# Kernel tuning notes

Measured on AMD Instinct MI355X. Metric: run time of the kernel, lower is better.

## Reference

```python
import jax, jax.numpy as jnp
import numpy as np

N, E, D, L = 50000, 640000, 128, 3  # nodes, edges, channels, layers
EPS = 1e-5


def setup_inputs() -> dict:
    key = jax.random.key(0)
    ks = jax.random.split(key, 10)
    s = 1.0 / np.sqrt(D)
    inp = {
        "x": jax.random.normal(ks[0], (N, D), dtype=jnp.float32),
        "edge_attr": jax.random.normal(ks[1], (E, D), dtype=jnp.float32),
        "w_self": jax.random.normal(ks[2], (L, D, D), dtype=jnp.float32) * s,
        "b_self": jnp.zeros((L, D), dtype=jnp.float32),
        "w_in": jax.random.normal(ks[3], (L, D, D), dtype=jnp.float32) * s,
        "b_in": jnp.zeros((L, D), dtype=jnp.float32),
        "w_rel": jax.random.normal(ks[4], (L, D, D), dtype=jnp.float32) * s,
        "b_rel": jnp.zeros((L, D), dtype=jnp.float32),
        "bn_gamma": jnp.ones((L - 1, D), dtype=jnp.float32),
        "bn_beta": jnp.zeros((L - 1, D), dtype=jnp.float32),
        "edge_index": jax.random.randint(ks[5], (2, E), 0, N, dtype=jnp.int64),
    }
    return inp


def _batchnorm(h, gamma, beta):
    mu = jnp.mean(h, axis=0)
    var = jnp.mean(jnp.square(h - mu), axis=0)  # biased var (torch BN training)
    return (h - mu) * jax.lax.rsqrt(var + EPS) * gamma + beta


def reference(x, edge_attr, w_self, b_self, w_in, b_in, w_rel, b_rel,
              bn_gamma, bn_beta, edge_index):
    src, dst = edge_index[0], edge_index[1]
    # per-node in-degree for mean aggregation (zero-degree nodes -> 0)
    cnt = jax.ops.segment_sum(jnp.ones((E, 1), x.dtype), dst, num_segments=N)
    denom = jnp.maximum(cnt, 1.0)
    for i in range(L):
        # message: lin_in(x_j * edge_attr)
        msg = jnp.einsum('ed,fd->ef', x[src] * edge_attr, w_in[i]) + b_in[i]
        agg = jax.ops.segment_sum(msg, dst, num_segments=N) / denom  # scatter-mean
        x = agg + jnp.einsum('nd,fd->nf', x, w_self[i]) + b_self[i]
        edge_attr = jnp.einsum('ed,fd->ef', edge_attr, w_rel[i]) + b_rel[i]
        if i < L - 1:
            x = jax.nn.relu(_batchnorm(x, bn_gamma[i], bn_beta[i]))
            # dropout p=0.0 -> identity
    return (x, edge_attr)
```

## Files before the change

kernel.cpp:

```cpp
#include <hip/hip_runtime.h>

#define DD 128

typedef __attribute__((ext_vector_type(8))) short bf16x8;
typedef __attribute__((ext_vector_type(4))) short bf16x4;
typedef __attribute__((ext_vector_type(4))) float f32x4;
typedef unsigned short u16;

__device__ __forceinline__ unsigned short f2bf(float f) {
  union { float f; unsigned u; } v; v.f = f;
  unsigned u = v.u;
  return (unsigned short)((u + 0x7FFFu + ((u >> 16) & 1u)) >> 16);
}
__device__ __forceinline__ float bf2f(unsigned short h) {
  union { unsigned u; float f; } v; v.u = ((unsigned)h) << 16; return v.f;
}

__device__ __forceinline__ bf16x8 pack8(f32x4 a, f32x4 b) {
  bf16x8 r;
  r[0] = (short)f2bf(a.x); r[1] = (short)f2bf(a.y);
  r[2] = (short)f2bf(a.z); r[3] = (short)f2bf(a.w);
  r[4] = (short)f2bf(b.x); r[5] = (short)f2bf(b.y);
  r[6] = (short)f2bf(b.z); r[7] = (short)f2bf(b.w);
  return r;
}

__device__ __forceinline__ bool idx_is64(const int* p) {
  return (p[1] | p[3] | p[5] | p[7]) == 0;
}
__device__ __forceinline__ int ld_idx(const int* p, long long i, bool is64) {
  return is64 ? (int)((const long long*)p)[i] : p[i];
}

__global__ void k_count(const int* __restrict__ idx, int* __restrict__ cnt, int E) {
  int e = blockIdx.x * blockDim.x + threadIdx.x;
  if (e >= E) return;
  bool is64 = idx_is64(idx);
  int d = ld_idx(idx, (long long)E + e, is64);
  atomicAdd(&cnt[d], 1);
}

__global__ __launch_bounds__(1024) void k_scan(const int* __restrict__ cnt,
    int* __restrict__ row_start, int* __restrict__ cursor, int N) {
  __shared__ int part[1024];
  int t = threadIdx.x;
  int chunk = (N + 1023) >> 10;
  int lo = t * chunk, hi = lo + chunk; if (hi > N) hi = N; if (lo > N) lo = N;
  int s = 0;
  for (int i = lo; i < hi; ++i) s += cnt[i];
  part[t] = s;
  __syncthreads();
  for (int off = 1; off < 1024; off <<= 1) {
    int v = (t >= off) ? part[t - off] : 0;
    __syncthreads();
    part[t] += v;
    __syncthreads();
  }
  int run = (t == 0) ? 0 : part[t - 1];
  for (int i = lo; i < hi; ++i) {
    row_start[i] = run; cursor[i] = run; run += cnt[i];
  }
  if (t == 1023) row_start[N] = part[1023];
}

__global__ void k_fill(const int* __restrict__ idx, int* __restrict__ cursor,
                       int* __restrict__ edge_of, int* __restrict__ src_csr, int E) {
  int e = blockIdx.x * blockDim.x + threadIdx.x;
  if (e >= E) return;
  bool is64 = idx_is64(idx);
  int s = ld_idx(idx, e, is64);
  int d = ld_idx(idx, (long long)E + e, is64);
  int pos = atomicAdd(&cursor[d], 1);
  edge_of[pos] = e;
  src_csr[pos] = s;
}

__global__ __launch_bounds__(256) void k_agg0(const float* __restrict__ x,
    const float* __restrict__ ea, const int* __restrict__ edge_of,
    const int* __restrict__ src_csr, const int* __restrict__ row_start,
    float* __restrict__ aggm, u16* __restrict__ eaC) {
  int n = blockIdx.x * 4 + (threadIdx.x >> 6);
  int lane = threadIdx.x & 63;
  int esub = lane >> 4, cg = lane & 15;
  int c0 = cg * 8;
  int s0 = row_start[n], s1 = row_start[n + 1];
  int len = s1 - s0;
  float acc[8];
#pragma unroll
  for (int j = 0; j < 8; ++j) acc[j] = 0.f;
  for (int kk = 0; kk < len; kk += 4) {
    int kx = kk + esub;
    bool act = kx < len;
    int k = s0 + (act ? kx : 0);
    int e = edge_of[k];
    int sn = src_csr[k];
    f32x4 e0 = *(const f32x4*)(ea + (size_t)e * DD + c0);
    f32x4 e1 = *(const f32x4*)(ea + (size_t)e * DD + c0 + 4);
    f32x4 x0 = *(const f32x4*)(x + (size_t)sn * DD + c0);
    f32x4 x1 = *(const f32x4*)(x + (size_t)sn * DD + c0 + 4);
    if (act) {
      *(bf16x8*)(eaC + (size_t)k * DD + c0) = pack8(e0, e1);
#pragma unroll
      for (int j = 0; j < 4; ++j) acc[j] += x0[j] * e0[j];
#pragma unroll
      for (int j = 0; j < 4; ++j) acc[4 + j] += x1[j] * e1[j];
    }
  }
  float inv = (len > 0) ? 1.0f / (float)len : 0.0f;
#pragma unroll
  for (int j = 0; j < 8; ++j) {
    float s = acc[j];
    s += __shfl_xor(s, 16);
    s += __shfl_xor(s, 32);
    acc[j] = s * inv;
  }
  if (esub == 0) {
    f32x4 lo, hi;
#pragma unroll
    for (int j = 0; j < 4; ++j) { lo[j] = acc[j]; hi[j] = acc[4 + j]; }
    *(f32x4*)(aggm + (size_t)n * DD + c0) = lo;
    *(f32x4*)(aggm + (size_t)n * DD + c0 + 4) = hi;
  }
}

__global__ __launch_bounds__(256) void k_aggN(const u16* __restrict__ xb,
    const u16* __restrict__ eaC, const int* __restrict__ src_csr,
    const int* __restrict__ row_start, const float* __restrict__ scale,
    const float* __restrict__ shift, float* __restrict__ aggm) {
  int n = blockIdx.x * 4 + (threadIdx.x >> 6);
  int lane = threadIdx.x & 63;
  int esub = lane >> 4, cg = lane & 15;
  int c0 = cg * 8;
  float sc[8], sh[8];
#pragma unroll
  for (int j = 0; j < 8; ++j) { sc[j] = scale[c0 + j]; sh[j] = shift[c0 + j]; }
  int s0 = row_start[n], s1 = row_start[n + 1];
  int len = s1 - s0;
  float acc[8];
#pragma unroll
  for (int j = 0; j < 8; ++j) acc[j] = 0.f;
  for (int kk = 0; kk < len; kk += 4) {
    int kx = kk + esub;
    bool act = kx < len;
    int k = s0 + (act ? kx : 0);
    int sn = src_csr[k];
    bf16x8 ev = *(const bf16x8*)(eaC + (size_t)k * DD + c0);
    bf16x8 xv = *(const bf16x8*)(xb + (size_t)sn * DD + c0);
    if (act) {
#pragma unroll
      for (int j = 0; j < 8; ++j) {
        float xf = fmaxf(bf2f((u16)xv[j]) * sc[j] + sh[j], 0.f);
        acc[j] += xf * bf2f((u16)ev[j]);
      }
    }
  }
  float inv = (len > 0) ? 1.0f / (float)len : 0.0f;
#pragma unroll
  for (int j = 0; j < 8; ++j) {
    float s = acc[j];
    s += __shfl_xor(s, 16);
    s += __shfl_xor(s, 32);
    acc[j] = s * inv;
  }
  if (esub == 0) {
    f32x4 lo, hi;
#pragma unroll
    for (int j = 0; j < 4; ++j) { lo[j] = acc[j]; hi[j] = acc[4 + j]; }
    *(f32x4*)(aggm + (size_t)n * DD + c0) = lo;
    *(f32x4*)(aggm + (size_t)n * DD + c0 + 4) = hi;
  }
}

template <typename TX, bool BN, typename TO, bool STATS>
__global__ __launch_bounds__(256) void k_node(const float* __restrict__ aggm,
    const TX* __restrict__ xc, const float* __restrict__ W_in,
    const float* __restrict__ W_self, const float* __restrict__ b_in,
    const float* __restrict__ b_self, const int* __restrict__ row_start,
    const float* __restrict__ scale, const float* __restrict__ shift,
    TO* __restrict__ xn, float* __restrict__ gsum, float* __restrict__ gssq,
    int ntiles) {
  __shared__ short Wl[DD * 256];
  for (int q = threadIdx.x; q < DD * 256 / 4; q += 256) {
    int off = q * 4;
    int f = off >> 8, k = off & 255;
    f32x4 w = (k < 128) ? *(const f32x4*)(W_in + f * 128 + k)
                        : *(const f32x4*)(W_self + f * 128 + (k - 128));
    unsigned byte = ((unsigned)(f * 512 + k * 2)) ^ (unsigned)((f & 7) << 4);
    bf16x4 s4;
    s4[0] = (short)f2bf(w.x); s4[1] = (short)f2bf(w.y);
    s4[2] = (short)f2bf(w.z); s4[3] = (short)f2bf(w.w);
    *(bf16x4*)((char*)Wl + byte) = s4;
  }
  __syncthreads();
  int wave = threadIdx.x >> 6, lane = threadIdx.x & 63;
  int tile = blockIdx.x * 4 + wave;
  if (tile >= ntiles) return;
  int r = lane & 15, g = lane >> 4;
  int arowi = tile * 16 + r;
  const float* arow = aggm + (size_t)arowi * DD;
  const TX* xrow = xc + (size_t)arowi * DD;
  bf16x8 a[8];
#pragma unroll
  for (int ks = 0; ks < 4; ++ks) {
    const float* p = arow + ks * 32 + g * 8;
    a[ks] = pack8(*(const f32x4*)p, *(const f32x4*)(p + 4));
  }
#pragma unroll
  for (int ks = 0; ks < 4; ++ks) {
    int c0 = ks * 32 + g * 8;
    float v[8];
    if constexpr (sizeof(TX) == 2) {
      bf16x8 raw = *(const bf16x8*)(xrow + c0);
#pragma unroll
      for (int j = 0; j < 8; ++j) v[j] = bf2f((u16)raw[j]);
    } else {
      f32x4 r0 = *(const f32x4*)((const float*)xrow + c0);
      f32x4 r1 = *(const f32x4*)((const float*)xrow + c0 + 4);
#pragma unroll
      for (int j = 0; j < 4; ++j) { v[j] = r0[j]; v[4 + j] = r1[j]; }
    }
    bf16x8 fr;
#pragma unroll
    for (int j = 0; j < 8; ++j) {
      float f = v[j];
      if constexpr (BN) f = fmaxf(f * scale[c0 + j] + shift[c0 + j], 0.f);
      fr[j] = (short)f2bf(f);
    }
    a[4 + ks] = fr;
  }
  f32x4 acc[8];
#pragma unroll
  for (int ct = 0; ct < 8; ++ct) acc[ct] = (f32x4){0.f, 0.f, 0.f, 0.f};
#pragma unroll
  for (int ct = 0; ct < 8; ++ct) {
    int f = ct * 16 + r;
    unsigned base = (unsigned)(f * 512);
    unsigned sw = (unsigned)((f & 7) << 4);
#pragma unroll
    for (int ks = 0; ks < 8; ++ks) {
      unsigned byte = (base + (unsigned)(ks * 64 + g * 16)) ^ sw;
      bf16x8 b = *(const bf16x8*)((const char*)Wl + byte);
      acc[ct] = __builtin_amdgcn_mfma_f32_16x16x32_bf16(a[ks], b, acc[ct], 0, 0, 0);
    }
  }
  int nbase = tile * 16;
  float degmask[4];
#pragma unroll
  for (int j = 0; j < 4; ++j) {
    int nn = nbase + g * 4 + j;
    degmask[j] = (row_start[nn + 1] > row_start[nn]) ? 1.0f : 0.0f;
  }
#pragma unroll
  for (int ct = 0; ct < 8; ++ct) {
    int col = ct * 16 + r;
    float bi = b_in[col], bs = b_self[col];
    float s = 0.f, s2 = 0.f;
#pragma unroll
    for (int j = 0; j < 4; ++j) {
      float v = acc[ct][j] + bs + bi * degmask[j];
      if constexpr (sizeof(TO) == 2) xn[(size_t)(nbase + g * 4 + j) * DD + col] = (TO)f2bf(v);
      else                            xn[(size_t)(nbase + g * 4 + j) * DD + col] = (TO)v;
      s += v; s2 += v * v;
    }
    if constexpr (STATS) {
      s += __shfl_xor(s, 16);  s += __shfl_xor(s, 32);
      s2 += __shfl_xor(s2, 16); s2 += __shfl_xor(s2, 32);
      if (g == 0) { atomicAdd(&gsum[col], s); atomicAdd(&gssq[col], s2); }
    }
  }
}

template <bool SCATTER, typename TO>
__global__ __launch_bounds__(256) void k_rel(const u16* __restrict__ ea_in,
    TO* __restrict__ ea_out, const int* __restrict__ edge_of,
    const float* __restrict__ W, const float* __restrict__ bias, int ntiles) {
  __shared__ short Wl[DD * DD];
  for (int q = threadIdx.x; q < DD * DD / 4; q += 256) {
    int off = q * 4;
    int f = off >> 7, d = off & 127;
    f32x4 w = *(const f32x4*)(W + off);
    unsigned byte = ((unsigned)(f * 256 + d * 2)) ^ (unsigned)((f & 7) << 4);
    bf16x4 s4;
    s4[0] = (short)f2bf(w.x); s4[1] = (short)f2bf(w.y);
    s4[2] = (short)f2bf(w.z); s4[3] = (short)f2bf(w.w);
    *(bf16x4*)((char*)Wl + byte) = s4;
  }
  __syncthreads();
  int wave = threadIdx.x >> 6, lane = threadIdx.x & 63;
  int r = lane & 15, g = lane >> 4;
  for (int tile = blockIdx.x * 4 + wave; tile < ntiles; tile += gridDim.x * 4) {
    const u16* rowp = ea_in + (size_t)(tile * 16 + r) * DD;
    bf16x8 a[4];
#pragma unroll
    for (int ks = 0; ks < 4; ++ks) a[ks] = *(const bf16x8*)(rowp + ks * 32 + g * 8);
    f32x4 acc[8];
#pragma unroll
    for (int ct = 0; ct < 8; ++ct) acc[ct] = (f32x4){0.f, 0.f, 0.f, 0.f};
#pragma unroll
    for (int ct = 0; ct < 8; ++ct) {
      int f = ct * 16 + r;
      unsigned base = (unsigned)(f * 256);
      unsigned sw = (unsigned)((f & 7) << 4);
#pragma unroll
      for (int ks = 0; ks < 4; ++ks) {
        unsigned byte = (base + (unsigned)(ks * 64 + g * 16)) ^ sw;
        bf16x8 b = *(const bf16x8*)((const char*)Wl + byte);
        acc[ct] = __builtin_amdgcn_mfma_f32_16x16x32_bf16(a[ks], b, acc[ct], 0, 0, 0);
      }
    }
    size_t orow[4];
#pragma unroll
    for (int j = 0; j < 4; ++j) {
      int kr = tile * 16 + g * 4 + j;
      orow[j] = SCATTER ? (size_t)edge_of[kr] : (size_t)kr;
    }
#pragma unroll
    for (int ct = 0; ct < 8; ++ct) {
      int col = ct * 16 + r;
      float bv = bias[col];
#pragma unroll
      for (int j = 0; j < 4; ++j) {
        float v = acc[ct][j] + bv;
        if constexpr (sizeof(TO) == 2) ea_out[orow[j] * DD + col] = (TO)f2bf(v);
        else                            ea_out[orow[j] * DD + col] = (TO)v;
      }
    }
  }
}

__global__ void k_bnfin(const float* __restrict__ gsum, const float* __restrict__ gssq,
    const float* __restrict__ gamma, const float* __restrict__ beta,
    float* __restrict__ scale, float* __restrict__ shift, int N) {
  int d = threadIdx.x;
  float mu = gsum[d] / (float)N;
  float var = gssq[d] / (float)N - mu * mu;
  float rs = rsqrtf(var + 1e-5f);
  float sc = rs * gamma[d];
  scale[d] = sc;
  shift[d] = beta[d] - mu * sc;
}

static inline size_t alignup(size_t v, size_t a) { return (v + a - 1) & ~(a - 1); }

extern "C" void kernel_launch(void* const* d_in, const int* in_sizes, int n_in,
                              void* d_out, int out_size, void* d_ws, size_t ws_size,
                              hipStream_t stream) {
  const float* x0     = (const float*)d_in[0];
  const float* ea0    = (const float*)d_in[1];
  const float* w_self = (const float*)d_in[2];
  const float* b_self = (const float*)d_in[3];
  const float* w_in   = (const float*)d_in[4];
  const float* b_in   = (const float*)d_in[5];
  const float* w_rel  = (const float*)d_in[6];
  const float* b_rel  = (const float*)d_in[7];
  const float* gamma  = (const float*)d_in[8];
  const float* beta   = (const float*)d_in[9];
  const int*   idx    = (const int*)d_in[10];

  const int N = in_sizes[0] / DD;
  const int E = in_sizes[1] / DD;

  char* w = (char*)d_ws;
  size_t off = 0;
  int* cnt       = (int*)(w + off); off = alignup(off + (size_t)N * 4, 256);
  int* row_start = (int*)(w + off); off = alignup(off + (size_t)(N + 1) * 4, 256);
  int* cursor    = (int*)(w + off); off = alignup(off + (size_t)N * 4, 256);
  int* edge_of   = (int*)(w + off); off = alignup(off + (size_t)E * 4, 256);
  int* src_csr   = (int*)(w + off); off = alignup(off + (size_t)E * 4, 256);
  float* gstats  = (float*)(w + off); off = alignup(off + 256 * 4, 256);
  float* scale   = (float*)(w + off); off = alignup(off + 128 * 4, 256);
  float* shift   = (float*)(w + off); off = alignup(off + 128 * 4, 256);
  float* aggm    = (float*)(w + off); off = alignup(off + (size_t)N * DD * 4, 256);
  u16*   xb      = (u16*)(w + off);   off = alignup(off + (size_t)N * DD * 2, 256);
  u16*   eaC     = (u16*)(w + off);   off = alignup(off + (size_t)E * DD * 2, 256);
  float* gsum = gstats, *gssq = gstats + 128;
  (void)ws_size; (void)n_in; (void)out_size;

  float* out_x  = (float*)d_out;
  float* out_ea = out_x + (size_t)N * DD;

  (void)hipMemsetAsync(cnt, 0, (size_t)N * 4, stream);
  int ethreads = 256, eblocks = (E + ethreads - 1) / ethreads;
  k_count<<<eblocks, ethreads, 0, stream>>>(idx, cnt, E);
  k_scan<<<1, 1024, 0, stream>>>(cnt, row_start, cursor, N);
  k_fill<<<eblocks, ethreads, 0, stream>>>(idx, cursor, edge_of, src_csr, E);

  const int ntN = N / 16;
  const int ntE = E / 16;
  const int aggBlocks = (N + 3) / 4;
  const int nodeBlocks = (ntN + 3) / 4;
  const int relBlocks = 2048;

  (void)hipMemsetAsync(gstats, 0, 256 * 4, stream);
  k_agg0<<<aggBlocks, 256, 0, stream>>>(x0, ea0, edge_of, src_csr, row_start,
                                        aggm, eaC);
  k_node<float, false, u16, true><<<nodeBlocks, 256, 0, stream>>>(aggm, x0,
      w_in, w_self, b_in, b_self, row_start, scale, shift,
      xb, gsum, gssq, ntN);
  k_rel<false, u16><<<relBlocks, 256, 0, stream>>>(eaC, eaC, edge_of,
      w_rel, b_rel, ntE);
  k_bnfin<<<1, 128, 0, stream>>>(gsum, gssq, gamma, beta, scale, shift, N);

  (void)hipMemsetAsync(gstats, 0, 256 * 4, stream);
  k_aggN<<<aggBlocks, 256, 0, stream>>>(xb, eaC, src_csr, row_start,
                                        scale, shift, aggm);
  k_node<u16, true, u16, true><<<nodeBlocks, 256, 0, stream>>>(aggm, xb,
      w_in + DD * DD, w_self + DD * DD, b_in + DD, b_self + DD,
      row_start, scale, shift, xb, gsum, gssq, ntN);
  k_rel<false, u16><<<relBlocks, 256, 0, stream>>>(eaC, eaC, edge_of,
      w_rel + DD * DD, b_rel + DD, ntE);
  k_bnfin<<<1, 128, 0, stream>>>(gsum, gssq, gamma + DD, beta + DD, scale, shift, N);

  k_aggN<<<aggBlocks, 256, 0, stream>>>(xb, eaC, src_csr, row_start,
                                        scale, shift, aggm);
  k_node<u16, true, float, false><<<nodeBlocks, 256, 0, stream>>>(aggm, xb,
      w_in + 2 * DD * DD, w_self + 2 * DD * DD, b_in + 2 * DD, b_self + 2 * DD,
      row_start, scale, shift, out_x, gsum, gssq, ntN);
  k_rel<true, float><<<relBlocks, 256, 0, stream>>>(eaC, out_ea, edge_of,
      w_rel + 2 * DD * DD, b_rel + 2 * DD, ntE);
}
```

Baseline: 1.030 ms.

## Fuse aggregation, node update and edge transform into one per-layer kernel

Each layer's gather-aggregation, node GEMM and edge-attribute GEMM now run in a single kernel. One in five blocks does aggregation plus the node MFMA, with the aggregate kept in LDS as bf16 instead of a global fp32 buffer. The other blocks run the edge transform concurrently, writing through an inverse permutation so layer 0 lands in CSR order. Edge and node buffers are double-buffered, and the BN stat reset moves into k_bnfin to drop the memsets. This removes kernel launches and the aggm round trip, but each aggregating wave now handles 16 nodes serially, which risks load imbalance and less parallelism in the gather phase.

Result: slower. 1.103 ms (+7.2%).

```diff
diff --git a/kernel.cpp b/kernel.cpp
--- a/kernel.cpp
+++ b/kernel.cpp
@@ -15,7 +15,6 @@
 __device__ __forceinline__ float bf2f(unsigned short h) {
   union { unsigned u; float f; } v; v.u = ((unsigned)h) << 16; return v.f;
 }
-
 __device__ __forceinline__ bf16x8 pack8(f32x4 a, f32x4 b) {
   bf16x8 r;
   r[0] = (short)f2bf(a.x); r[1] = (short)f2bf(a.y);
@@ -64,7 +63,8 @@
 }
 
 __global__ void k_fill(const int* __restrict__ idx, int* __restrict__ cursor,
-                       int* __restrict__ edge_of, int* __restrict__ src_csr, int E) {
+                       int* __restrict__ edge_of, int* __restrict__ src_csr,
+                       int* __restrict__ inv, int E) {
   int e = blockIdx.x * blockDim.x + threadIdx.x;
   if (e >= E) return;
   bool is64 = idx_is64(idx);
@@ -73,262 +73,232 @@
   int pos = atomicAdd(&cursor[d], 1);
   edge_of[pos] = e;
   src_csr[pos] = s;
-}
-
-__global__ __launch_bounds__(256) void k_agg0(const float* __restrict__ x,
-    const float* __restrict__ ea, const int* __restrict__ edge_of,
-    const int* __restrict__ src_csr, const int* __restrict__ row_start,
-    float* __restrict__ aggm, u16* __restrict__ eaC) {
-  int n = blockIdx.x * 4 + (threadIdx.x >> 6);
-  int lane = threadIdx.x & 63;
-  int esub = lane >> 4, cg = lane & 15;
-  int c0 = cg * 8;
-  int s0 = row_start[n], s1 = row_start[n + 1];
-  int len = s1 - s0;
-  float acc[8];
-#pragma unroll
-  for (int j = 0; j < 8; ++j) acc[j] = 0.f;
-  for (int kk = 0; kk < len; kk += 4) {
-    int kx = kk + esub;
-    bool act = kx < len;
-    int k = s0 + (act ? kx : 0);
-    int e = edge_of[k];
-    int sn = src_csr[k];
-    f32x4 e0 = *(const f32x4*)(ea + (size_t)e * DD + c0);
-    f32x4 e1 = *(const f32x4*)(ea + (size_t)e * DD + c0 + 4);
-    f32x4 x0 = *(const f32x4*)(x + (size_t)sn * DD + c0);
-    f32x4 x1 = *(const f32x4*)(x + (size_t)sn * DD + c0 + 4);
-    if (act) {
-      *(bf16x8*)(eaC + (size_t)k * DD + c0) = pack8(e0, e1);
-#pragma unroll
-      for (int j = 0; j < 4; ++j) acc[j] += x0[j] * e0[j];
-#pragma unroll
-      for (int j = 0; j < 4; ++j) acc[4 + j] += x1[j] * e1[j];
-    }
-  }
-  float inv = (len > 0) ? 1.0f / (float)len : 0.0f;
-#pragma unroll
-  for (int j = 0; j < 8; ++j) {
-    float s = acc[j];
-    s += __shfl_xor(s, 16);
-    s += __shfl_xor(s, 32);
-    acc[j] = s * inv;
-  }
-  if (esub == 0) {
-    f32x4 lo, hi;
-#pragma unroll
-    for (int j = 0; j < 4; ++j) { lo[j] = acc[j]; hi[j] = acc[4 + j]; }
-    *(f32x4*)(aggm + (size_t)n * DD + c0) = lo;
-    *(f32x4*)(aggm + (size_t)n * DD + c0 + 4) = hi;
-  }
-}
-
-__global__ __launch_bounds__(256) void k_aggN(const u16* __restrict__ xb,
-    const u16* __restrict__ eaC, const int* __restrict__ src_csr,
-    const int* __restrict__ row_start, const float* __restrict__ scale,
-    const float* __restrict__ shift, float* __restrict__ aggm) {
-  int n = blockIdx.x * 4 + (threadIdx.x >> 6);
-  int lane = threadIdx.x & 63;
-  int esub = lane >> 4, cg = lane & 15;
-  int c0 = cg * 8;
-  float sc[8], sh[8];
-#pragma unroll
-  for (int j = 0; j < 8; ++j) { sc[j] = scale[c0 + j]; sh[j] = shift[c0 + j]; }
-  int s0 = row_start[n], s1 = row_start[n + 1];
-  int len = s1 - s0;
-  float acc[8];
-#pragma unroll
-  for (int j = 0; j < 8; ++j) acc[j] = 0.f;
-  for (int kk = 0; kk < len; kk += 4) {
-    int kx = kk + esub;
-    bool act = kx < len;
-    int k = s0 + (act ? kx : 0);
-    int sn = src_csr[k];
-    bf16x8 ev = *(const bf16x8*)(eaC + (size_t)k * DD + c0);
-    bf16x8 xv = *(const bf16x8*)(xb + (size_t)sn * DD + c0);
-    if (act) {
+  inv[e] = pos;
+}
+
+template <int MODE>
+__global__ __launch_bounds__(256) void k_layer(
+    const float* __restrict__ x0, const u16* __restrict__ xbin,
+    const float* __restrict__ ea0, const u16* __restrict__ eain,
+    u16* __restrict__ xbout, float* __restrict__ xfout,
+    u16* __restrict__ eabout, float* __restrict__ eafout,
+    const int* __restrict__ row_start, const int* __restrict__ edge_of,
+    const int* __restrict__ src_csr, const int* __restrict__ inv,
+    const float* __restrict__ w_in, const float* __restrict__ w_self,
+    const float* __restrict__ b_in, const float* __restrict__ b_self,
+    const float* __restrict__ w_rel, const float* __restrict__ b_rel,
+    const float* __restrict__ scale, const float* __restrict__ shift,
+    float* __restrict__ gsum, float* __restrict__ gssq,
+    int ntN, int ntE, int strideB) {
+  __shared__ short LDS[40960];
+  int bid = blockIdx.x;
+  int tid = threadIdx.x;
+  int wave = tid >> 6, lane = tid & 63;
+  bool isA = (bid % 5) == 4;
+
+  if (isA) {
+    for (int q = tid; q < 8192; q += 256) {
+      int off = q * 4;
+      int f = off >> 8, k = off & 255;
+      f32x4 w = (k < 128) ? *(const f32x4*)(w_in + f * 128 + k)
+                          : *(const f32x4*)(w_self + f * 128 + (k - 128));
+      unsigned byte = ((unsigned)(f * 512 + k * 2)) ^ (unsigned)((f & 7) << 4);
+      bf16x4 s4;
+      s4[0] = (short)f2bf(w.x); s4[1] = (short)f2bf(w.y);
+      s4[2] = (short)f2bf(w.z); s4[3] = (short)f2bf(w.w);
+      *(bf16x4*)((char*)LDS + byte) = s4;
+    }
+    __syncthreads();
+    int tile = (bid / 5) * 4 + wave;
+    if (tile >= ntN) return;
+    short* aggL = LDS + 32768 + wave * 2048;
+    int esub = lane >> 4, cg = lane & 15;
+    int c0g = cg * 8;
+    float scA[8], shA[8];
+    if constexpr (MODE >= 1) {
+#pragma unroll
+      for (int j = 0; j < 8; ++j) { scA[j] = scale[c0g + j]; shA[j] = shift[c0g + j]; }
+    }
+    for (int n16 = 0; n16 < 16; ++n16) {
+      int n = tile * 16 + n16;
+      int s0 = row_start[n], s1 = row_start[n + 1];
+      int len = s1 - s0;
+      float acc[8];
+#pragma unroll
+      for (int j = 0; j < 8; ++j) acc[j] = 0.f;
+      for (int kk = 0; kk < len; kk += 4) {
+        int kx = kk + esub;
+        bool act = kx < len;
+        int k = s0 + (act ? kx : 0);
+        if constexpr (MODE == 0) {
+          int e = edge_of[k];
+          int sn = src_csr[k];
+          const float* ep = ea0 + (size_t)e * DD + c0g;
+          f32x4 e0 = *(const f32x4*)ep, e1 = *(const f32x4*)(ep + 4);
+          const float* xp = x0 + (size_t)sn * DD + c0g;
+          f32x4 xv0 = *(const f32x4*)xp, xv1 = *(const f32x4*)(xp + 4);
+          if (act) {
+#pragma unroll
+            for (int j = 0; j < 4; ++j) { acc[j] += xv0[j] * e0[j]; acc[4 + j] += xv1[j] * e1[j]; }
+          }
+        } else {
+          int sn = src_csr[k];
+          bf16x8 ev = *(const bf16x8*)(eain + (size_t)k * DD + c0g);
+          bf16x8 xv = *(const bf16x8*)(xbin + (size_t)sn * DD + c0g);
+          if (act) {
+#pragma unroll
+            for (int j = 0; j < 8; ++j) {
+              float xf = fmaxf(bf2f((u16)xv[j]) * scA[j] + shA[j], 0.f);
+              acc[j] += xf * bf2f((u16)ev[j]);
+            }
+          }
+        }
+      }
+      float invd = (len > 0) ? 1.0f / (float)len : 0.0f;
 #pragma unroll
       for (int j = 0; j < 8; ++j) {
-        float xf = fmaxf(bf2f((u16)xv[j]) * sc[j] + sh[j], 0.f);
-        acc[j] += xf * bf2f((u16)ev[j]);
-      }
-    }
-  }
-  float inv = (len > 0) ? 1.0f / (float)len : 0.0f;
-#pragma unroll
-  for (int j = 0; j < 8; ++j) {
-    float s = acc[j];
-    s += __shfl_xor(s, 16);
-    s += __shfl_xor(s, 32);
-    acc[j] = s * inv;
-  }
-  if (esub == 0) {
-    f32x4 lo, hi;
-#pragma unroll
-    for (int j = 0; j < 4; ++j) { lo[j] = acc[j]; hi[j] = acc[4 + j]; }
-    *(f32x4*)(aggm + (size_t)n * DD + c0) = lo;
-    *(f32x4*)(aggm + (size_t)n * DD + c0 + 4) = hi;
-  }
-}
-
-template <typename TX, bool BN, typename TO, bool STATS>
-__global__ __launch_bounds__(256) void k_node(const float* __restrict__ aggm,
-    const TX* __restrict__ xc, const float* __restrict__ W_in,
-    const float* __restrict__ W_self, const float* __restrict__ b_in,
-    const float* __restrict__ b_self, const int* __restrict__ row_start,
-    const float* __restrict__ scale, const float* __restrict__ shift,
-    TO* __restrict__ xn, float* __restrict__ gsum, float* __restrict__ gssq,
-    int ntiles) {
-  __shared__ short Wl[DD * 256];
-  for (int q = threadIdx.x; q < DD * 256 / 4; q += 256) {
-    int off = q * 4;
-    int f = off >> 8, k = off & 255;
-    f32x4 w = (k < 128) ? *(const f32x4*)(W_in + f * 128 + k)
-                        : *(const f32x4*)(W_self + f * 128 + (k - 128));
-    unsigned byte = ((unsigned)(f * 512 + k * 2)) ^ (unsigned)((f & 7) << 4);
-    bf16x4 s4;
-    s4[0] = (short)f2bf(w.x); s4[1] = (short)f2bf(w.y);
-    s4[2] = (short)f2bf(w.z); s4[3] = (short)f2bf(w.w);
-    *(bf16x4*)((char*)Wl + byte) = s4;
-  }
-  __syncthreads();
-  int wave = threadIdx.x >> 6, lane = threadIdx.x & 63;
-  int tile = blockIdx.x * 4 + wave;
-  if (tile >= ntiles) return;
-  int r = lane & 15, g = lane >> 4;
-  int arowi = tile * 16 + r;
-  const float* arow = aggm + (size_t)arowi * DD;
-  const TX* xrow = xc + (size_t)arowi * DD;
-  bf16x8 a[8];
-#pragma unroll
-  for (int ks = 0; ks < 4; ++ks) {
-    const float* p = arow + ks * 32 + g * 8;
-    a[ks] = pack8(*(const f32x4*)p, *(const f32x4*)(p + 4));
-  }
-#pragma unroll
-  for (int ks = 0; ks < 4; ++ks) {
-    int c0 = ks * 32 + g * 8;
-    float v[8];
-    if constexpr (sizeof(TX) == 2) {
-      bf16x8 raw = *(const bf16x8*)(xrow + c0);
-#pragma unroll
-      for (int j = 0; j < 8; ++j) v[j] = bf2f((u16)raw[j]);
-    } else {
-      f32x4 r0 = *(const f32x4*)((const float*)xrow + c0);
-      f32x4 r1 = *(const f32x4*)((const float*)xrow + c0 + 4);
-#pragma unroll
-      for (int j = 0; j < 4; ++j) { v[j] = r0[j]; v[4 + j] = r1[j]; }
-    }
-    bf16x8 fr;
-#pragma unroll
-    for (int j = 0; j < 8; ++j) {
-      float f = v[j];
-      if constexpr (BN) f = fmaxf(f * scale[c0 + j] + shift[c0 + j], 0.f);
-      fr[j] = (short)f2bf(f);
-    }
-    a[4 + ks] = fr;
-  }
-  f32x4 acc[8];
-#pragma unroll
-  for (int ct = 0; ct < 8; ++ct) acc[ct] = (f32x4){0.f, 0.f, 0.f, 0.f};
-#pragma unroll
-  for (int ct = 0; ct < 8; ++ct) {
-    int f = ct * 16 + r;
-    unsigned base = (unsigned)(f * 512);
-    unsigned sw = (unsigned)((f & 7) << 4);
-#pragma unroll
-    for (int ks = 0; ks < 8; ++ks) {
-      unsigned byte = (base + (unsigned)(ks * 64 + g * 16)) ^ sw;
-      bf16x8 b = *(const bf16x8*)((const char*)Wl + byte);
-      acc[ct] = __builtin_amdgcn_mfma_f32_16x16x32_bf16(a[ks], b, acc[ct], 0, 0, 0);
-    }
-  }
-  int nbase = tile * 16;
-  float degmask[4];
-#pragma unroll
-  for (int j = 0; j < 4; ++j) {
-    int nn = nbase + g * 4 + j;
-    degmask[j] = (row_start[nn + 1] > row_start[nn]) ? 1.0f : 0.0f;
-  }
-#pragma unroll
-  for (int ct = 0; ct < 8; ++ct) {
-    int col = ct * 16 + r;
-    float bi = b_in[col], bs = b_self[col];
-    float s = 0.f, s2 = 0.f;
-#pragma unroll
-    for (int j = 0; j < 4; ++j) {
-      float v = acc[ct][j] + bs + bi * degmask[j];
-      if constexpr (sizeof(TO) == 2) xn[(size_t)(nbase + g * 4 + j) * DD + col] = (TO)f2bf(v);
-      else                            xn[(size_t)(nbase + g * 4 + j) * DD + col] = (TO)v;
-      s += v; s2 += v * v;
-    }
-    if constexpr (STATS) {
-      s += __shfl_xor(s, 16);  s += __shfl_xor(s, 32);
-      s2 += __shfl_xor(s2, 16); s2 += __shfl_xor(s2, 32);
-      if (g == 0) { atomicAdd(&gsum[col], s); atomicAdd(&gssq[col], s2); }
-    }
-  }
-}
-
-template <bool SCATTER, typename TO>
-__global__ __launch_bounds__(256) void k_rel(const u16* __restrict__ ea_in,
-    TO* __restrict__ ea_out, const int* __restrict__ edge_of,
-    const float* __restrict__ W, const float* __restrict__ bias, int ntiles) {
-  __shared__ short Wl[DD * DD];
-  for (int q = threadIdx.x; q < DD * DD / 4; q += 256) {
-    int off = q * 4;
-    int f = off >> 7, d = off & 127;
-    f32x4 w = *(const f32x4*)(W + off);
-    unsigned byte = ((unsigned)(f * 256 + d * 2)) ^ (unsigned)((f & 7) << 4);
-    bf16x4 s4;
-    s4[0] = (short)f2bf(w.x); s4[1] = (short)f2bf(w.y);
-    s4[2] = (short)f2bf(w.z); s4[3] = (short)f2bf(w.w);
-    *(bf16x4*)((char*)Wl + byte) = s4;
-  }
-  __syncthreads();
-  int wave = threadIdx.x >> 6, lane = threadIdx.x & 63;
-  int r = lane & 15, g = lane >> 4;
-  for (int tile = blockIdx.x * 4 + wave; tile < ntiles; tile += gridDim.x * 4) {
-    const u16* rowp = ea_in + (size_t)(tile * 16 + r) * DD;
-    bf16x8 a[4];
-#pragma unroll
-    for (int ks = 0; ks < 4; ++ks) a[ks] = *(const bf16x8*)(rowp + ks * 32 + g * 8);
-    f32x4 acc[8];
-#pragma unroll
-    for (int ct = 0; ct < 8; ++ct) acc[ct] = (f32x4){0.f, 0.f, 0.f, 0.f};
+        float s = acc[j];
+        s += __shfl_xor(s, 16);
+        s += __shfl_xor(s, 32);
+        acc[j] = s * invd;
+      }
+      if (esub == 0) {
+        f32x4 lo, hi;
+#pragma unroll
+        for (int j = 0; j < 4; ++j) { lo[j] = acc[j]; hi[j] = acc[4 + j]; }
+        *(bf16x8*)(aggL + n16 * 128 + ((cg ^ (n16 & 15)) * 8)) = pack8(lo, hi);
+      }
+    }
+    asm volatile("s_waitcnt lgkmcnt(0)" ::: "memory");
+    int r = lane & 15, g = lane >> 4;
+    bf16x8 a8[8];
+#pragma unroll
+    for (int ks = 0; ks < 4; ++ks)
+      a8[ks] = *(const bf16x8*)(aggL + r * 128 + (((ks * 4 + g) ^ (r & 15)) * 8));
+#pragma unroll
+    for (int ks = 0; ks < 4; ++ks) {
+      int c0 = ks * 32 + g * 8;
+      if constexpr (MODE == 0) {
+        const float* p = x0 + (size_t)(tile * 16 + r) * DD + c0;
+        a8[4 + ks] = pack8(*(const f32x4*)p, *(const f32x4*)(p + 4));
+      } else {
+        bf16x8 raw = *(const bf16x8*)(xbin + (size_t)(tile * 16 + r) * DD + c0);
+        bf16x8 fr;
+#pragma unroll
+        for (int j = 0; j < 8; ++j) {
+          float f = fmaxf(bf2f((u16)raw[j]) * scale[c0 + j] + shift[c0 + j], 0.f);
+          fr[j] = (short)f2bf(f);
+        }
+        a8[4 + ks] = fr;
+      }
+    }
+    f32x4 acc4[8];
+#pragma unroll
+    for (int ct = 0; ct < 8; ++ct) acc4[ct] = (f32x4){0.f, 0.f, 0.f, 0.f};
 #pragma unroll
     for (int ct = 0; ct < 8; ++ct) {
       int f = ct * 16 + r;
-      unsigned base = (unsigned)(f * 256);
+      unsigned base = (unsigned)(f * 512);
       unsigned sw = (unsigned)((f & 7) << 4);
 #pragma unroll
-      for (int ks = 0; ks < 4; ++ks) {
+      for (int ks = 0; ks < 8; ++ks) {
         unsigned byte = (base + (unsigned)(ks * 64 + g * 16)) ^ sw;
-        bf16x8 b = *(const bf16x8*)((const char*)Wl + byte);
-        acc[ct] = __builtin_amdgcn_mfma_f32_16x16x32_bf16(a[ks], b, acc[ct], 0, 0, 0);
-      }
-    }
-    size_t orow[4];
+        bf16x8 b = *(const bf16x8*)((const char*)LDS + byte);
+        acc4[ct] = __builtin_amdgcn_mfma_f32_16x16x32_bf16(a8[ks], b, acc4[ct], 0, 0, 0);
+      }
+    }
+    int nbase = tile * 16;
+    float degmask[4];
 #pragma unroll
     for (int j = 0; j < 4; ++j) {
-      int kr = tile * 16 + g * 4 + j;
-      orow[j] = SCATTER ? (size_t)edge_of[kr] : (size_t)kr;
+      int nn = nbase + g * 4 + j;
+      degmask[j] = (row_start[nn + 1] > row_start[nn]) ? 1.0f : 0.0f;
     }
 #pragma unroll
     for (int ct = 0; ct < 8; ++ct) {
       int col = ct * 16 + r;
-      float bv = bias[col];
+      float bi = b_in[col], bs = b_self[col];
+      float s = 0.f, s2 = 0.f;
 #pragma unroll
       for (int j = 0; j < 4; ++j) {
-        float v = acc[ct][j] + bv;
-        if constexpr (sizeof(TO) == 2) ea_out[orow[j] * DD + col] = (TO)f2bf(v);
-        else                            ea_out[orow[j] * DD + col] = (TO)v;
+        float v = acc4[ct][j] + bs + bi * degmask[j];
+        if constexpr (MODE < 2) xbout[(size_t)(nbase + g * 4 + j) * DD + col] = f2bf(v);
+        else                    xfout[(size_t)(nbase + g * 4 + j) * DD + col] = v;
+        s += v; s2 += v * v;
+      }
+      if constexpr (MODE < 2) {
+        s += __shfl_xor(s, 16);  s += __shfl_xor(s, 32);
+        s2 += __shfl_xor(s2, 16); s2 += __shfl_xor(s2, 32);
+        if (g == 0) { atomicAdd(&gsum[col], s); atomicAdd(&gssq[col], s2); }
+      }
+    }
+  } else {
+    int b = bid - (bid + 1) / 5;
+    for (int q = tid; q < 4096; q += 256) {
+      int off = q * 4;
+      int f = off >> 7, d = off & 127;
+      f32x4 w = *(const f32x4*)(w_rel + off);
+      unsigned byte = ((unsigned)(f * 256 + d * 2)) ^ (unsigned)((f & 7) << 4);
+      bf16x4 s4;
+      s4[0] = (short)f2bf(w.x); s4[1] = (short)f2bf(w.y);
+      s4[2] = (short)f2bf(w.z); s4[3] = (short)f2bf(w.w);
+      *(bf16x4*)((char*)LDS + byte) = s4;
+    }
+    __syncthreads();
+    int r = lane & 15, g = lane >> 4;
+    for (int tile = b * 4 + wave; tile < ntE; tile += strideB) {
+      bf16x8 a8[4];
+      if constexpr (MODE == 0) {
+        const float* rp = ea0 + (size_t)(tile * 16 + r) * DD;
+#pragma unroll
+        for (int ks = 0; ks < 4; ++ks) {
+          const float* p = rp + ks * 32 + g * 8;
+          a8[ks] = pack8(*(const f32x4*)p, *(const f32x4*)(p + 4));
+        }
+      } else {
+        const u16* rp = eain + (size_t)(tile * 16 + r) * DD;
+#pragma unroll
+        for (int ks = 0; ks < 4; ++ks) a8[ks] = *(const bf16x8*)(rp + ks * 32 + g * 8);
+      }
+      f32x4 acc4[8];
+#pragma unroll
+      for (int ct = 0; ct < 8; ++ct) acc4[ct] = (f32x4){0.f, 0.f, 0.f, 0.f};
+#pragma unroll
+      for (int ct = 0; ct < 8; ++ct) {
+        int f = ct * 16 + r;
+        unsigned base = (unsigned)(f * 256);
+        unsigned sw = (unsigned)((f & 7) << 4);
+#pragma unroll
+        for (int ks = 0; ks < 4; ++ks) {
+          unsigned byte = (base + (unsigned)(ks * 64 + g * 16)) ^ sw;
+          bf16x8 bb = *(const bf16x8*)((const char*)LDS + byte);
+          acc4[ct] = __builtin_amdgcn_mfma_f32_16x16x32_bf16(a8[ks], bb, acc4[ct], 0, 0, 0);
+        }
+      }
+      size_t orow[4];
+#pragma unroll
+      for (int j = 0; j < 4; ++j) {
+        int kr = tile * 16 + g * 4 + j;
+        if constexpr (MODE == 0)      orow[j] = (size_t)inv[kr];
+        else if constexpr (MODE == 1) orow[j] = (size_t)kr;
+        else                          orow[j] = (size_t)edge_of[kr];
+      }
+#pragma unroll
+      for (int ct = 0; ct < 8; ++ct) {
+        int col = ct * 16 + r;
+        float bv = b_rel[col];
+#pragma unroll
+        for (int j = 0; j < 4; ++j) {
+          float v = acc4[ct][j] + bv;
+          if constexpr (MODE == 2) eafout[orow[j] * DD + col] = v;
+          else                     eabout[orow[j] * DD + col] = f2bf(v);
+        }
       }
     }
   }
 }
 
-__global__ void k_bnfin(const float* __restrict__ gsum, const float* __restrict__ gssq,
+__global__ void k_bnfin(float* __restrict__ gsum, float* __restrict__ gssq,
     const float* __restrict__ gamma, const float* __restrict__ beta,
     float* __restrict__ scale, float* __restrict__ shift, int N) {
   int d = threadIdx.x;
@@ -338,6 +308,8 @@
   float sc = rs * gamma[d];
   scale[d] = sc;
   shift[d] = beta[d] - mu * sc;
+  gsum[d] = 0.f;
+  gssq[d] = 0.f;
 }
 
 static inline size_t alignup(size_t v, size_t a) { return (v + a - 1) & ~(a - 1); }
@@ -367,12 +339,14 @@
   int* cursor    = (int*)(w + off); off = alignup(off + (size_t)N * 4, 256);
   int* edge_of   = (int*)(w + off); off = alignup(off + (size_t)E * 4, 256);
   int* src_csr   = (int*)(w + off); off = alignup(off + (size_t)E * 4, 256);
+  int* inv       = (int*)(w + off); off = alignup(off + (size_t)E * 4, 256);
   float* gstats  = (float*)(w + off); off = alignup(off + 256 * 4, 256);
   float* scale   = (float*)(w + off); off = alignup(off + 128 * 4, 256);
   float* shift   = (float*)(w + off); off = alignup(off + 128 * 4, 256);
-  float* aggm    = (float*)(w + off); off = alignup(off + (size_t)N * DD * 4, 256);
-  u16*   xb      = (u16*)(w + off);   off = alignup(off + (size_t)N * DD * 2, 256);
-  u16*   eaC     = (u16*)(w + off);   off = alignup(off + (size_t)E * DD * 2, 256);
+  u16* xbA       = (u16*)(w + off); off = alignup(off + (size_t)N * DD * 2, 256);
+  u16* xbB       = (u16*)(w + off); off = alignup(off + (size_t)N * DD * 2, 256);
+  u16* eaA       = (u16*)(w + off); off = alignup(off + (size_t)E * DD * 2, 256);
+  u16* eaB       = (u16*)(w + off); off = alignup(off + (size_t)E * DD * 2, 256);
   float* gsum = gstats, *gssq = gstats + 128;
   (void)ws_size; (void)n_in; (void)out_size;
 
@@ -383,39 +357,34 @@
   int ethreads = 256, eblocks = (E + ethreads - 1) / ethreads;
   k_count<<<eblocks, ethreads, 0, stream>>>(idx, cnt, E);
   k_scan<<<1, 1024, 0, stream>>>(cnt, row_start, cursor, N);
-  k_fill<<<eblocks, ethreads, 0, stream>>>(idx, cursor, edge_of, src_csr, E);
+  k_fill<<<eblocks, ethreads, 0, stream>>>(idx, cursor, edge_of, src_csr, inv, E);
+  (void)hipMemsetAsync(gstats, 0, 256 * 4, stream);
 
   const int ntN = N / 16;
   const int ntE = E / 16;
-  const int aggBlocks = (N + 3) / 4;
-  const int nodeBlocks = (ntN + 3) / 4;
-  const int relBlocks = 2048;
-
-  (void)hipMemsetAsync(gstats, 0, 256 * 4, stream);
-  k_agg0<<<aggBlocks, 256, 0, stream>>>(x0, ea0, edge_of, src_csr, row_start,
-                                        aggm, eaC);
-  k_node<float, false, u16, true><<<nodeBlocks, 256, 0, stream>>>(aggm, x0,
-      w_in, w_self, b_in, b_self, row_start, scale, shift,
-      xb, gsum, gssq, ntN);
-  k_rel<false, u16><<<relBlocks, 256, 0, stream>>>(eaC, eaC, edge_of,
-      w_rel, b_rel, ntE);
+  const int nA = (ntN + 3) / 4;
+  const int grid = nA * 5;
+  const int strideB = (grid - nA) * 4;
+
+  k_layer<0><<<grid, 256, 0, stream>>>(x0, nullptr, ea0, nullptr,
+      xbA, nullptr, eaA, nullptr,
+      row_start, edge_of, src_csr, inv,
+      w_in, w_self, b_in, b_self, w_rel, b_rel,
+      scale, shift, gsum, gssq, ntN, ntE, strideB);
   k_bnfin<<<1, 128, 0, stream>>>(gsum, gssq, gamma, beta, scale, shift, N);
 
-  (void)hipMemsetAsync(gstats, 0, 256 * 4, stream);
-  k_aggN<<<aggBlocks, 256, 0, stream>>>(xb, eaC, src_csr, row_start,
-                                        scale, shift, aggm);
-  k_node<u16, true, u16, true><<<nodeBlocks, 256, 0, stream>>>(aggm, xb,
+  k_layer<1><<<grid, 256, 0, stream>>>(nullptr, xbA, nullptr, eaA,
+      xbB, nullptr, eaB, nullptr,
+      row_start, edge_of, src_csr, inv,
       w_in + DD * DD, w_self + DD * DD, b_in + DD, b_self + DD,
-      row_start, scale, shift, xb, gsum, gssq, ntN);
-  k_rel<false, u16><<<relBlocks, 256, 0, stream>>>(eaC, eaC, edge_of,
-      w_rel + DD * DD, b_rel + DD, ntE);
+      w_rel + DD * DD, b_rel + DD,
+      scale, shift, gsum, gssq, ntN, ntE, strideB);
   k_bnfin<<<1, 128, 0, stream>>>(gsum, gssq, gamma + DD, beta + DD, scale, shift, N);
 
-  k_aggN<<<aggBlocks, 256, 0, stream>>>(xb, eaC, src_csr, row_start,
-                                        scale, shift, aggm);
-  k_node<u16, true, float, false><<<nodeBlocks, 256, 0, stream>>>(aggm, xb,
+  k_layer<2><<<grid, 256, 0, stream>>>(nullptr, xbB, nullptr, eaB,
+      nullptr, out_x, nullptr, out_ea,
+      row_start, edge_of, src_csr, inv,
       w_in + 2 * DD * DD, w_self + 2 * DD * DD, b_in + 2 * DD, b_self + 2 * DD,
-      row_start, scale, shift, out_x, gsum, gssq, ntN);
-  k_rel<true, float><<<relBlocks, 256, 0, stream>>>(eaC, out_ea, edge_of,
-      w_rel + 2 * DD * DD, b_rel + 2 * DD, ntE);
-}
+      w_rel + 2 * DD * DD, b_rel + 2 * DD,
+      scale, shift, gsum, gssq, ntN, ntE, strideB);
+}
```
